# Kernel tuning notes

Hardware: AMD Instinct MI355X
Metric: run time of the kernel (lower is better)

The kernel has to match this reference:

```python
import jax, jax.numpy as jnp
import numpy as np

B, S, D, H = 4, 2048, 1024, 16
DK = D // H

def setup_inputs() -> dict:
    key = jax.random.key(0)
    ks = jax.random.split(key, 11)
    scale = 1.0 / np.sqrt(D)
    return {
        "query": jax.random.normal(ks[0], (B, S, D), jnp.float32),
        "key_": jax.random.normal(ks[1], (B, S, D), jnp.float32),
        "value": jax.random.normal(ks[2], (B, S, D), jnp.float32),
        "Wq": jax.random.normal(ks[3], (D, D), jnp.float32) * scale,
        "bq": jnp.zeros((D,), jnp.float32),
        "Wk": jax.random.normal(ks[4], (D, D), jnp.float32) * scale,
        "bk": jnp.zeros((D,), jnp.float32),
        "Wv": jax.random.normal(ks[5], (D, D), jnp.float32) * scale,
        "bv": jnp.zeros((D,), jnp.float32),
        "Wo": jax.random.normal(ks[6], (D, D), jnp.float32) * scale,
        "bo": jnp.zeros((D,), jnp.float32),
    }

def reference(query, key_, value, Wq, bq, Wk, bk, Wv, bv, Wo, bo):
    # Linear projections (torch Linear: x @ W.T + b)
    Q = query @ Wq.T + bq            # [B,S,D]
    K = key_ @ Wk.T + bk
    V = value @ Wv.T + bv
    # split heads -> [B,H,S,DK]
    def split(x):
        return x.reshape(B, S, H, DK).transpose(0, 2, 1, 3)
    Qh, Kh, Vh = split(Q), split(K), split(V)
    scores = jnp.einsum("bhqd,bhkd->bhqk", Qh, Kh) / np.sqrt(DK)
    attn = jax.nn.softmax(scores, axis=-1)
    ctx = jnp.einsum("bhqk,bhkd->bhqd", attn, Vh)
    ctx = ctx.transpose(0, 2, 1, 3).reshape(B, S, D)
    return ctx @ Wo.T + bo
```

## Files before the change

### kernel.cpp

```cpp
#include <hip/hip_runtime.h>
#include <hip/hip_bf16.h>
#include <stdint.h>

#define B_ 4
#define S_ 2048
#define D_ 1024
#define H_ 16
#define DK_ 64
#define GM (B_ * S_)
#define GN D_
#define GK D_
#define BM 128
#define BN 128
#define BK 64
#define QBLK 128

typedef __attribute__((ext_vector_type(8))) __bf16 bf16x8;
typedef __attribute__((ext_vector_type(4))) float f32x4;
typedef __attribute__((ext_vector_type(4))) uint32_t u32x4;

#if __has_builtin(__builtin_amdgcn_exp2f)
#define EXP2F(x) __builtin_amdgcn_exp2f(x)
#else
#define EXP2F(x) exp2f(x)
#endif

#define SCALE_LOG2E 0.18033688011112042f

__device__ __forceinline__ uint16_t f2bf(float x) {
  uint32_t u = __builtin_bit_cast(uint32_t, x);
  u += 0x7fffu + ((u >> 16) & 1u);
  return (uint16_t)(u >> 16);
}
__device__ __forceinline__ void gload_lds16(const void* g, void* l) {
  __builtin_amdgcn_global_load_lds(
      (const __attribute__((address_space(1))) void*)g,
      (__attribute__((address_space(3))) void*)l, 16, 0, 0);
}

__device__ __forceinline__ int swzK(int kv, int colb) {
  return colb ^ ((kv & 7) << 4);
}
__device__ __forceinline__ int swzV(int dk, int off) {
  return off ^ ((((dk >> 3) ^ dk) & 7) << 4);
}
__device__ __forceinline__ int swzP(int q, int off) {
  return off ^ ((q & 7) << 4) ^ (((q >> 2) & 3) << 5);
}

struct CvtArgs {
  const float* src[7];
  uint16_t* dst[7];
  int n[7];
  float scale[7];
};

__global__ __launch_bounds__(256) void cvt_f32_bf16(CvtArgs a) {
  const int z = blockIdx.z;
  const float* __restrict__ s = a.src[z];
  uint16_t* __restrict__ d = a.dst[z];
  const float sc = a.scale[z];
  const int nv = a.n[z] >> 3;
  const int stride = gridDim.x * blockDim.x;
  for (int i = blockIdx.x * blockDim.x + threadIdx.x; i < nv; i += stride) {
    f32x4 v0 = *(const f32x4*)(s + (size_t)i * 8);
    f32x4 v1 = *(const f32x4*)(s + (size_t)i * 8 + 4);
    union { uint16_t u[8]; u32x4 q; } o;
#pragma unroll
    for (int j = 0; j < 4; ++j) o.u[j] = f2bf(v0[j] * sc);
#pragma unroll
    for (int j = 0; j < 4; ++j) o.u[4 + j] = f2bf(v1[j] * sc);
    *(u32x4*)(d + (size_t)i * 8) = o.q;
  }
}

struct Gemm3Args {
  const uint16_t* A[3];
  const uint16_t* W[3];
  const float* bias[3];
  float bscale[3];
  void* C[3];
};

template <bool CF32>
__global__ __launch_bounds__(256, 2) void mha_gemm3(Gemm3Args args) {
  const int z = blockIdx.z;
  const char* __restrict__ A = (const char*)args.A[z];
  const char* __restrict__ W = (const char*)args.W[z];
  const float* __restrict__ bias = args.bias[z];
  const float bsc = args.bscale[z];
  void* __restrict__ C = args.C[z];

  __shared__ alignas(16) uint16_t tA[BM][BK];
  __shared__ alignas(16) uint16_t tW[BN][BK];

  const int tid = threadIdx.x;
  const int lane = tid & 63;
  const int wid = tid >> 6;
  const int wm = wid >> 1, wn = wid & 1;
  const int l16 = lane & 15, g = lane >> 4;

  const int m0 = blockIdx.y * BM;
  const int n0 = blockIdx.x * BN;

  f32x4 acc[4][4] = {};
  const int o = tid * 16;

  for (int k0 = 0; k0 < GK; k0 += BK) {
#pragma unroll
    for (int i = 0; i < 4; ++i) {
      const int oo = o + i * 4096;
      const int row = oo >> 7, colb = oo & 127;
      gload_lds16(A + (size_t)(m0 + row) * (GK * 2) + (size_t)k0 * 2 + colb,
                  ((char*)&tA[0][0]) + i * 4096 + wid * 1024);
      gload_lds16(W + (size_t)(n0 + row) * (GK * 2) + (size_t)k0 * 2 + colb,
                  ((char*)&tW[0][0]) + i * 4096 + wid * 1024);
    }
    __syncthreads();
#pragma unroll
    for (int kk = 0; kk < 2; ++kk) {
      const int kcol = kk * 32 + g * 8;
      bf16x8 af[4], bfr[4];
#pragma unroll
      for (int m = 0; m < 4; ++m)
        af[m] = *(const bf16x8*)&tA[wm * 64 + m * 16 + l16][kcol];
#pragma unroll
      for (int n = 0; n < 4; ++n)
        bfr[n] = *(const bf16x8*)&tW[wn * 64 + n * 16 + l16][kcol];
#pragma unroll
      for (int m = 0; m < 4; ++m)
#pragma unroll
        for (int n = 0; n < 4; ++n)
          acc[m][n] = __builtin_amdgcn_mfma_f32_16x16x32_bf16(
              af[m], bfr[n], acc[m][n], 0, 0, 0);
    }
    __syncthreads();
  }

#pragma unroll
  for (int n = 0; n < 4; ++n) {
    const int col = n0 + wn * 64 + n * 16 + l16;
    const float bv = bias[col] * bsc;
#pragma unroll
    for (int m = 0; m < 4; ++m) {
      const int rbase = m0 + wm * 64 + m * 16 + g * 4;
#pragma unroll
      for (int r = 0; r < 4; ++r) {
        const float v = acc[m][n][r] + bv;
        if (CF32)
          ((float*)C)[(size_t)(rbase + r) * GN + col] = v;
        else
          ((uint16_t*)C)[(size_t)(rbase + r) * GN + col] = f2bf(v);
      }
    }
  }
}

__global__ __launch_bounds__(256) void mha_attn(
    const uint16_t* __restrict__ Q, const uint16_t* __restrict__ K,
    const uint16_t* __restrict__ V, uint16_t* __restrict__ O) {
  __shared__ alignas(16) char K_s[2][64 * 128];
  __shared__ alignas(16) char V_s[2][64 * 128];
  __shared__ alignas(16) char P_s[4 * 32 * 128];

  const int tid = threadIdx.x;
  const int lane = tid & 63;
  const int wid = tid >> 6;
  const int l16 = lane & 15, g = lane >> 4;
  const int bh = blockIdx.y;
  const int b = bh >> 4, h = bh & 15;
  const int q0 = blockIdx.x * QBLK;

  bf16x8 qf[2][2];
#pragma unroll
  for (int mi = 0; mi < 2; ++mi) {
    const uint16_t* qp = Q + ((size_t)(b * S_) + q0 + mi * 64 + wid * 16 + l16) * D_ +
                         h * DK_ + g * 8;
    qf[mi][0] = *(const bf16x8*)qp;
    qf[mi][1] = *(const bf16x8*)(qp + 32);
  }

  f32x4 o_acc[2][4] = {};
  float lpart[2][4] = {};

  const char* Kb = (const char*)K;
  const char* Vb = (const char*)V;
  const size_t rowb = (size_t)D_ * 2;
  const size_t headoff = (size_t)h * DK_ * 2;
  char* P_w = P_s + wid * 4096;

  int srow[2], scolb[2];
#pragma unroll
  for (int i = 0; i < 2; ++i) {
    const int oo = tid * 16 + i * 4096;
    srow[i] = oo >> 7;
    scolb[i] = oo & 127;
  }

#define ISSUE_LOADS(buf, kv0, vreg)                                            \
  {                                                                            \
    _Pragma("unroll") for (int i = 0; i < 2; ++i) {                            \
      const size_t base = ((size_t)(b * S_) + (kv0) + srow[i]) * rowb + headoff;\
      gload_lds16(Kb + base + (scolb[i] ^ ((srow[i] & 7) << 4)),               \
                  &K_s[buf][0] + i * 4096 + wid * 1024);                       \
      vreg[i] = *(const u32x4*)(Vb + base + scolb[i]);                         \
    }                                                                          \
  }

#define WRITE_V(buf, vreg)                                                     \
  {                                                                            \
    _Pragma("unroll") for (int i = 0; i < 2; ++i) {                            \
      const int c0 = scolb[i] >> 1;                                            \
      _Pragma("unroll") for (int j = 0; j < 4; ++j) {                          \
        const uint32_t w = vreg[i][j];                                         \
        const int dk0 = c0 + 2 * j, dk1 = dk0 + 1;                             \
        *(uint16_t*)(&V_s[buf][0] + dk0 * 128 + swzV(dk0, srow[i] * 2)) =      \
            (uint16_t)(w & 0xffffu);                                           \
        *(uint16_t*)(&V_s[buf][0] + dk1 * 128 + swzV(dk1, srow[i] * 2)) =      \
            (uint16_t)(w >> 16);                                               \
      }                                                                        \
    }                                                                          \
  }

  u32x4 vreg[2];
  ISSUE_LOADS(0, 0, vreg);
  WRITE_V(0, vreg);
  __syncthreads();
  int cur = 0;

  for (int kv0 = 0; kv0 < S_; kv0 += 64) {
    const bool last = (kv0 + 64 >= S_);
    if (!last) ISSUE_LOADS(cur ^ 1, kv0 + 64, vreg);

    f32x4 sacc[2][4] = {};
#pragma unroll
    for (int ks = 0; ks < 2; ++ks) {
      const int kcolb = ks * 64 + g * 16;
#pragma unroll
      for (int n = 0; n < 4; ++n) {
        const int kvr = n * 16 + l16;
        const bf16x8 kf =
            *(const bf16x8*)(&K_s[cur][0] + kvr * 128 + swzK(kvr, kcolb));
#pragma unroll
        for (int mi = 0; mi < 2; ++mi)
          sacc[mi][n] = __builtin_amdgcn_mfma_f32_16x16x32_bf16(
              qf[mi][ks], kf, sacc[mi][n], 0, 0, 0);
      }
    }

#pragma unroll
    for (int mi = 0; mi < 2; ++mi)
#pragma unroll
      for (int n = 0; n < 4; ++n)
#pragma unroll
        for (int r = 0; r < 4; ++r) {
          const float p = EXP2F(sacc[mi][n][r]);
          lpart[mi][r] += p;
          const int q = mi * 16 + g * 4 + r;
          const int off = (n * 16 + l16) * 2;
          *(uint16_t*)(P_w + q * 128 + swzP(q, off)) = f2bf(p);
        }

#pragma unroll
    for (int ks = 0; ks < 2; ++ks) {
      const int kcolb = ks * 64 + g * 16;
      bf16x8 pf[2];
#pragma unroll
      for (int mi = 0; mi < 2; ++mi) {
        const int q = mi * 16 + l16;
        pf[mi] = *(const bf16x8*)(P_w + q * 128 + swzP(q, kcolb));
      }
#pragma unroll
      for (int n = 0; n < 4; ++n) {
        const int dk = n * 16 + l16;
        const bf16x8 vf =
            *(const bf16x8*)(&V_s[cur][0] + dk * 128 + swzV(dk, kcolb));
#pragma unroll
        for (int mi = 0; mi < 2; ++mi)
          o_acc[mi][n] = __builtin_amdgcn_mfma_f32_16x16x32_bf16(
              pf[mi], vf, o_acc[mi][n], 0, 0, 0);
      }
    }

    if (!last) {
      WRITE_V(cur ^ 1, vreg);
      __syncthreads();
    }
    cur ^= 1;
  }

  float linv[2][4];
#pragma unroll
  for (int mi = 0; mi < 2; ++mi)
#pragma unroll
    for (int r = 0; r < 4; ++r) {
      float s_ = lpart[mi][r];
#pragma unroll
      for (int msk = 1; msk < 16; msk <<= 1) s_ += __shfl_xor(s_, msk, 64);
      linv[mi][r] = 1.f / s_;
    }

#pragma unroll
  for (int mi = 0; mi < 2; ++mi) {
    const int qrow = q0 + mi * 64 + wid * 16 + g * 4;
#pragma unroll
    for (int n = 0; n < 4; ++n) {
      const int col = h * DK_ + n * 16 + l16;
#pragma unroll
      for (int r = 0; r < 4; ++r) {
        const float v = o_acc[mi][n][r] * linv[mi][r];
        O[((size_t)(b * S_) + qrow + r) * D_ + col] = f2bf(v);
      }
    }
  }
}

extern "C" void kernel_launch(void* const* d_in, const int* in_sizes, int n_in,
                              void* d_out, int out_size, void* d_ws,
                              size_t ws_size, hipStream_t stream) {
  (void)in_sizes; (void)n_in; (void)out_size; (void)ws_size;

  const float* query = (const float*)d_in[0];
  const float* key_ = (const float*)d_in[1];
  const float* value = (const float*)d_in[2];
  const float* Wq = (const float*)d_in[3];
  const float* bq = (const float*)d_in[4];
  const float* Wk = (const float*)d_in[5];
  const float* bk = (const float*)d_in[6];
  const float* Wv = (const float*)d_in[7];
  const float* bv = (const float*)d_in[8];
  const float* Wo = (const float*)d_in[9];
  const float* bo = (const float*)d_in[10];

  const size_t nact = (size_t)GM * GN;
  const size_t nw = (size_t)GN * GK;
  uint16_t* p = (uint16_t*)d_ws;
  uint16_t* qb = p; p += nact;
  uint16_t* kb = p; p += nact;
  uint16_t* vb = p; p += nact;
  uint16_t* wq = p; p += nw;
  uint16_t* wk = p; p += nw;
  uint16_t* wv = p; p += nw;
  uint16_t* wo = p; p += nw;
  uint16_t* Qp = p; p += nact;
  uint16_t* Kp = p; p += nact;
  uint16_t* Vp = p; p += nact;
  uint16_t* Cp = p; p += nact;

  CvtArgs ca;
  const float* srcs[7] = {query, key_, value, Wq, Wk, Wv, Wo};
  uint16_t* dsts[7] = {qb, kb, vb, wq, wk, wv, wo};
  const int cnts[7] = {(int)nact, (int)nact, (int)nact, (int)nw,
                       (int)nw,   (int)nw,   (int)nw};
  for (int i = 0; i < 7; ++i) {
    ca.src[i] = srcs[i]; ca.dst[i] = dsts[i]; ca.n[i] = cnts[i];
    ca.scale[i] = 1.0f;
  }
  ca.scale[3] = SCALE_LOG2E;
  cvt_f32_bf16<<<dim3(512, 1, 7), dim3(256), 0, stream>>>(ca);

  Gemm3Args g1;
  g1.A[0] = qb; g1.A[1] = kb; g1.A[2] = vb;
  g1.W[0] = wq; g1.W[1] = wk; g1.W[2] = wv;
  g1.bias[0] = bq; g1.bias[1] = bk; g1.bias[2] = bv;
  g1.bscale[0] = SCALE_LOG2E; g1.bscale[1] = 1.0f; g1.bscale[2] = 1.0f;
  g1.C[0] = Qp; g1.C[1] = Kp; g1.C[2] = Vp;
  mha_gemm3<false>
      <<<dim3(GN / BN, GM / BM, 3), dim3(256), 0, stream>>>(g1);

  mha_attn<<<dim3(S_ / QBLK, B_ * H_), dim3(256), 0, stream>>>(Qp, Kp, Vp, Cp);

  Gemm3Args g2;
  g2.A[0] = Cp; g2.W[0] = wo; g2.bias[0] = bo; g2.C[0] = d_out;
  g2.bscale[0] = 1.0f;
  g2.A[1] = g2.A[0]; g2.W[1] = g2.W[0]; g2.bias[1] = g2.bias[0]; g2.C[1] = g2.C[0];
  g2.bscale[1] = 1.0f;
  g2.A[2] = g2.A[0]; g2.W[2] = g2.W[0]; g2.bias[2] = g2.bias[0]; g2.C[2] = g2.C[0];
  g2.bscale[2] = 1.0f;
  mha_gemm3<true>
      <<<dim3(GN / BN, GM / BM, 1), dim3(256), 0, stream>>>(g2);
}
```

Measured before the change: 264.9 us.

## Pre-transpose V, keep P in registers via lane shuffles, pack bf16 output stores

Adds a separate kernel that transposes V per head into a [B,H,DK,S] buffer, which reuses the dead query bf16 buffer. The attention kernel can then load V tiles straight into LDS with async global_load_lds instead of scattering 2-byte transposed writes. The QK MFMA operands are swapped so the score layout matches the PV A-operand. P then stays in registers, packed with v_cvt_pk_bf16_f32 and redistributed by lane shuffles, which drops the P shared-memory round trip. The output is written as packed 8-byte stores. The cost is an extra kernel launch and a full read and write of V, plus the shuffle overhead.

```diff
diff --git a/kernel.cpp b/kernel.cpp
--- a/kernel.cpp
+++ b/kernel.cpp
@@ -18,6 +18,7 @@
 typedef __attribute__((ext_vector_type(8))) __bf16 bf16x8;
 typedef __attribute__((ext_vector_type(4))) float f32x4;
 typedef __attribute__((ext_vector_type(4))) uint32_t u32x4;
+typedef __attribute__((ext_vector_type(2))) uint32_t u32x2;
 
 #if __has_builtin(__builtin_amdgcn_exp2f)
 #define EXP2F(x) __builtin_amdgcn_exp2f(x)
@@ -32,20 +33,15 @@
   u += 0x7fffu + ((u >> 16) & 1u);
   return (uint16_t)(u >> 16);
 }
+__device__ __forceinline__ uint32_t cvtpk(float lo, float hi) {
+  uint32_t r;
+  asm("v_cvt_pk_bf16_f32 %0, %1, %2" : "=v"(r) : "v"(lo), "v"(hi));
+  return r;
+}
 __device__ __forceinline__ void gload_lds16(const void* g, void* l) {
   __builtin_amdgcn_global_load_lds(
       (const __attribute__((address_space(1))) void*)g,
       (__attribute__((address_space(3))) void*)l, 16, 0, 0);
-}
-
-__device__ __forceinline__ int swzK(int kv, int colb) {
-  return colb ^ ((kv & 7) << 4);
-}
-__device__ __forceinline__ int swzV(int dk, int off) {
-  return off ^ ((((dk >> 3) ^ dk) & 7) << 4);
-}
-__device__ __forceinline__ int swzP(int q, int off) {
-  return off ^ ((q & 7) << 4) ^ (((q >> 2) & 3) << 5);
 }
 
 struct CvtArgs {
@@ -156,12 +152,45 @@
   }
 }
 
+__global__ __launch_bounds__(256) void transpose_v(
+    const uint16_t* __restrict__ Vp, uint16_t* __restrict__ Vt) {
+  __shared__ alignas(16) char T[64 * 128];
+  const int tid = threadIdx.x;
+  const int s0 = blockIdx.x * 64;
+  const int h = blockIdx.y;
+  const int bb = blockIdx.z;
+#pragma unroll
+  for (int it = 0; it < 2; ++it) {
+    const int idx = tid + it * 256;
+    const int row = idx >> 3;
+    const int colb = (idx & 7) * 16;
+    const u32x4 v = *(const u32x4*)((const char*)Vp +
+        (((size_t)bb * S_ + s0 + row) * D_ + h * DK_) * 2 + colb);
+    *(u32x4*)(T + row * 128 + (colb ^ (((row >> 3) & 7) << 4))) = v;
+  }
+  __syncthreads();
+#pragma unroll
+  for (int it = 0; it < 2; ++it) {
+    const int idx = tid + it * 256;
+    const int dk = idx >> 3;
+    const int sc = (idx & 7) * 8;
+    union { uint16_t u[8]; u32x4 q; } o;
+#pragma unroll
+    for (int j = 0; j < 8; ++j) {
+      const int row = sc + j;
+      o.u[j] =
+          *(const uint16_t*)(T + row * 128 + ((dk * 2) ^ (((row >> 3) & 7) << 4)));
+    }
+    *(u32x4*)((char*)Vt +
+              (((size_t)(bb * H_ + h) * DK_ + dk) * S_ + s0 + sc) * 2) = o.q;
+  }
+}
+
 __global__ __launch_bounds__(256) void mha_attn(
     const uint16_t* __restrict__ Q, const uint16_t* __restrict__ K,
-    const uint16_t* __restrict__ V, uint16_t* __restrict__ O) {
-  __shared__ alignas(16) char K_s[2][64 * 128];
-  __shared__ alignas(16) char V_s[2][64 * 128];
-  __shared__ alignas(16) char P_s[4 * 32 * 128];
+    const uint16_t* __restrict__ Vt, uint16_t* __restrict__ O) {
+  __shared__ alignas(16) char K_s[2][8192];
+  __shared__ alignas(16) char V_s[2][8192];
 
   const int tid = threadIdx.x;
   const int lane = tid & 63;
@@ -181,56 +210,41 @@
   }
 
   f32x4 o_acc[2][4] = {};
-  float lpart[2][4] = {};
+  float lpart[2] = {0.f, 0.f};
 
   const char* Kb = (const char*)K;
-  const char* Vb = (const char*)V;
-  const size_t rowb = (size_t)D_ * 2;
-  const size_t headoff = (size_t)h * DK_ * 2;
-  char* P_w = P_s + wid * 4096;
-
-  int srow[2], scolb[2];
+  const char* Vtb = (const char*)Vt;
+
+  int srow[2], scol[2];
 #pragma unroll
   for (int i = 0; i < 2; ++i) {
     const int oo = tid * 16 + i * 4096;
     srow[i] = oo >> 7;
-    scolb[i] = oo & 127;
-  }
-
-#define ISSUE_LOADS(buf, kv0, vreg)                                            \
+    scol[i] = (oo & 127) ^ ((srow[i] & 7) << 4);
+  }
+
+#define ISSUE_LOADS(buf, kv0)                                                  \
   {                                                                            \
     _Pragma("unroll") for (int i = 0; i < 2; ++i) {                            \
-      const size_t base = ((size_t)(b * S_) + (kv0) + srow[i]) * rowb + headoff;\
-      gload_lds16(Kb + base + (scolb[i] ^ ((srow[i] & 7) << 4)),               \
+      gload_lds16(Kb + (((size_t)b * S_ + (kv0) + srow[i]) * D_ + h * DK_) * 2 \
+                      + scol[i],                                               \
                   &K_s[buf][0] + i * 4096 + wid * 1024);                       \
-      vreg[i] = *(const u32x4*)(Vb + base + scolb[i]);                         \
+      gload_lds16(Vtb + (((size_t)bh * DK_ + srow[i]) * S_ + (kv0)) * 2        \
+                      + scol[i],                                               \
+                  &V_s[buf][0] + i * 4096 + wid * 1024);                       \
     }                                                                          \
   }
 
-#define WRITE_V(buf, vreg)                                                     \
-  {                                                                            \
-    _Pragma("unroll") for (int i = 0; i < 2; ++i) {                            \
-      const int c0 = scolb[i] >> 1;                                            \
-      _Pragma("unroll") for (int j = 0; j < 4; ++j) {                          \
-        const uint32_t w = vreg[i][j];                                         \
-        const int dk0 = c0 + 2 * j, dk1 = dk0 + 1;                             \
-        *(uint16_t*)(&V_s[buf][0] + dk0 * 128 + swzV(dk0, srow[i] * 2)) =      \
-            (uint16_t)(w & 0xffffu);                                           \
-        *(uint16_t*)(&V_s[buf][0] + dk1 * 128 + swzV(dk1, srow[i] * 2)) =      \
-            (uint16_t)(w >> 16);                                               \
-      }                                                                        \
-    }                                                                          \
-  }
-
-  u32x4 vreg[2];
-  ISSUE_LOADS(0, 0, vreg);
-  WRITE_V(0, vreg);
+  ISSUE_LOADS(0, 0);
   __syncthreads();
   int cur = 0;
 
+  const int bsrc = l16 + ((g & 1) << 5);
+  const int gsel = g >> 1;
+
   for (int kv0 = 0; kv0 < S_; kv0 += 64) {
     const bool last = (kv0 + 64 >= S_);
-    if (!last) ISSUE_LOADS(cur ^ 1, kv0 + 64, vreg);
+    if (!last) ISSUE_LOADS(cur ^ 1, kv0 + 64);
 
     f32x4 sacc[2][4] = {};
 #pragma unroll
@@ -240,26 +254,38 @@
       for (int n = 0; n < 4; ++n) {
         const int kvr = n * 16 + l16;
         const bf16x8 kf =
-            *(const bf16x8*)(&K_s[cur][0] + kvr * 128 + swzK(kvr, kcolb));
+            *(const bf16x8*)(&K_s[cur][0] + kvr * 128 + (kcolb ^ ((kvr & 7) << 4)));
 #pragma unroll
         for (int mi = 0; mi < 2; ++mi)
           sacc[mi][n] = __builtin_amdgcn_mfma_f32_16x16x32_bf16(
-              qf[mi][ks], kf, sacc[mi][n], 0, 0, 0);
+              kf, qf[mi][ks], sacc[mi][n], 0, 0, 0);
       }
     }
 
-#pragma unroll
-    for (int mi = 0; mi < 2; ++mi)
-#pragma unroll
-      for (int n = 0; n < 4; ++n)
-#pragma unroll
-        for (int r = 0; r < 4; ++r) {
-          const float p = EXP2F(sacc[mi][n][r]);
-          lpart[mi][r] += p;
-          const int q = mi * 16 + g * 4 + r;
-          const int off = (n * 16 + l16) * 2;
-          *(uint16_t*)(P_w + q * 128 + swzP(q, off)) = f2bf(p);
+    uint32_t pb[2][2][4];
+#pragma unroll
+    for (int mi = 0; mi < 2; ++mi) {
+      uint32_t pk0[4][2];
+#pragma unroll
+      for (int n = 0; n < 4; ++n) {
+        float e0 = EXP2F(sacc[mi][n][0]);
+        float e1 = EXP2F(sacc[mi][n][1]);
+        float e2 = EXP2F(sacc[mi][n][2]);
+        float e3 = EXP2F(sacc[mi][n][3]);
+        lpart[mi] += (e0 + e1) + (e2 + e3);
+        pk0[n][0] = cvtpk(e0, e1);
+        pk0[n][1] = cvtpk(e2, e3);
+      }
+#pragma unroll
+      for (int ks = 0; ks < 2; ++ks)
+#pragma unroll
+        for (int jp = 0; jp < 4; ++jp) {
+          const int srcl = bsrc + ((jp >> 1) << 4);
+          const uint32_t va = __shfl(pk0[2 * ks][jp & 1], srcl, 64);
+          const uint32_t vb = __shfl(pk0[2 * ks + 1][jp & 1], srcl, 64);
+          pb[mi][ks][jp] = gsel ? vb : va;
         }
+    }
 
 #pragma unroll
     for (int ks = 0; ks < 2; ++ks) {
@@ -267,50 +293,43 @@
       bf16x8 pf[2];
 #pragma unroll
       for (int mi = 0; mi < 2; ++mi) {
-        const int q = mi * 16 + l16;
-        pf[mi] = *(const bf16x8*)(P_w + q * 128 + swzP(q, kcolb));
+        u32x4 t = {pb[mi][ks][0], pb[mi][ks][1], pb[mi][ks][2], pb[mi][ks][3]};
+        pf[mi] = __builtin_bit_cast(bf16x8, t);
       }
 #pragma unroll
       for (int n = 0; n < 4; ++n) {
-        const int dk = n * 16 + l16;
+        const int dkr = n * 16 + l16;
         const bf16x8 vf =
-            *(const bf16x8*)(&V_s[cur][0] + dk * 128 + swzV(dk, kcolb));
+            *(const bf16x8*)(&V_s[cur][0] + dkr * 128 + (kcolb ^ ((dkr & 7) << 4)));
 #pragma unroll
         for (int mi = 0; mi < 2; ++mi)
           o_acc[mi][n] = __builtin_amdgcn_mfma_f32_16x16x32_bf16(
-              pf[mi], vf, o_acc[mi][n], 0, 0, 0);
+              vf, pf[mi], o_acc[mi][n], 0, 0, 0);
       }
     }
 
-    if (!last) {
-      WRITE_V(cur ^ 1, vreg);
-      __syncthreads();
-    }
+    if (!last) __syncthreads();
     cur ^= 1;
   }
 
-  float linv[2][4];
-#pragma unroll
-  for (int mi = 0; mi < 2; ++mi)
-#pragma unroll
-    for (int r = 0; r < 4; ++r) {
-      float s_ = lpart[mi][r];
-#pragma unroll
-      for (int msk = 1; msk < 16; msk <<= 1) s_ += __shfl_xor(s_, msk, 64);
-      linv[mi][r] = 1.f / s_;
-    }
-
+  float linv[2];
 #pragma unroll
   for (int mi = 0; mi < 2; ++mi) {
-    const int qrow = q0 + mi * 64 + wid * 16 + g * 4;
+    float s_ = lpart[mi];
+    s_ += __shfl_xor(s_, 16, 64);
+    s_ += __shfl_xor(s_, 32, 64);
+    linv[mi] = 1.f / s_;
+  }
+#pragma unroll
+  for (int mi = 0; mi < 2; ++mi) {
+    const size_t row = (size_t)b * S_ + q0 + mi * 64 + wid * 16 + l16;
+    uint16_t* op = O + row * D_ + h * DK_ + g * 4;
 #pragma unroll
     for (int n = 0; n < 4; ++n) {
-      const int col = h * DK_ + n * 16 + l16;
-#pragma unroll
-      for (int r = 0; r < 4; ++r) {
-        const float v = o_acc[mi][n][r] * linv[mi][r];
-        O[((size_t)(b * S_) + qrow + r) * D_ + col] = f2bf(v);
-      }
+      u32x2 w;
+      w[0] = cvtpk(o_acc[mi][n][0] * linv[mi], o_acc[mi][n][1] * linv[mi]);
+      w[1] = cvtpk(o_acc[mi][n][2] * linv[mi], o_acc[mi][n][3] * linv[mi]);
+      *(u32x2*)(op + n * 16) = w;
     }
   }
 }
@@ -346,6 +365,7 @@
   uint16_t* Kp = p; p += nact;
   uint16_t* Vp = p; p += nact;
   uint16_t* Cp = p; p += nact;
+  uint16_t* Vt = qb;
 
   CvtArgs ca;
   const float* srcs[7] = {query, key_, value, Wq, Wk, Wv, Wo};
@@ -368,7 +388,9 @@
   mha_gemm3<false>
       <<<dim3(GN / BN, GM / BM, 3), dim3(256), 0, stream>>>(g1);
 
-  mha_attn<<<dim3(S_ / QBLK, B_ * H_), dim3(256), 0, stream>>>(Qp, Kp, Vp, Cp);
+  transpose_v<<<dim3(S_ / 64, H_, B_), dim3(256), 0, stream>>>(Vp, Vt);
+
+  mha_attn<<<dim3(S_ / QBLK, B_ * H_), dim3(256), 0, stream>>>(Qp, Kp, Vt, Cp);
 
   Gemm3Args g2;
   g2.A[0] = Cp; g2.W[0] = wo; g2.bias[0] = bo; g2.C[0] = d_out;
```

Result: no change. 267.7 us (+1.0%).
